# Kernel optimization log

Measured on AMD Instinct MI355X. Metric: run time of the kernel, lower is better.

Reference implementation:

```python
import jax, jax.numpy as jnp
import numpy as np

N_MODULES = 8
AG_HIDDEN = 512
N_HID = 512
OUT_SIZE = 10
BATCH = 8192


def _state_mask(n_modules, n0, n1):
    # torch: eye(M).repeat_interleave(n0, 0).repeat_interleave(n1, 1)
    m = jnp.eye(n_modules, dtype=jnp.float32)
    return jnp.repeat(jnp.repeat(m, n0, axis=0), n1, axis=1)


def setup_inputs() -> dict:
    key = jax.random.key(0)
    ks = jax.random.split(key, 5)
    d_in = N_MODULES * AG_HIDDEN
    d_hid = N_MODULES * N_HID
    d_out = N_MODULES * OUT_SIZE
    s1 = 1.0 / np.sqrt(d_in)
    s2 = 1.0 / np.sqrt(d_hid)
    return {
        "x": jax.random.normal(ks[0], (BATCH, d_in), jnp.float32),
        "W1": jax.random.uniform(ks[1], (d_hid, d_in), jnp.float32, -s1, s1),
        "b1": jax.random.uniform(ks[2], (d_hid,), jnp.float32, -s1, s1),
        "W2": jax.random.uniform(ks[3], (d_out, d_hid), jnp.float32, -s2, s2),
        "b2": jax.random.uniform(ks[4], (d_out,), jnp.float32, -s2, s2),
    }


def reference(x, W1, b1, W2, b2):
    # block-diagonal masks (intra-module connectivity only)
    mask1 = _state_mask(N_MODULES, N_HID, AG_HIDDEN)   # [d_hid, d_in]
    mask2 = _state_mask(N_MODULES, OUT_SIZE, N_HID)    # [d_out, d_hid]
    h = jax.nn.relu(x @ (W1 * mask1).T + b1)           # [B, d_hid]
    y = h @ (W2 * mask2).T + b2                        # [B, d_out]
    # split(OUT_SIZE, -1) then stack on dim 1 == reshape to [B, n_modules, OUT_SIZE]
    return y.reshape(y.shape[0], N_MODULES, OUT_SIZE)
```

## Files before the change

kernel.cpp:

```cpp
#include <hip/hip_runtime.h>


#define NMOD 8
#define DIM 512
#define OSZ 10
#define BATCH 8192
#define D_IN 4096
#define D_OUT 80
#define BM 64
#define BN 256
#define BK 32

typedef __attribute__((ext_vector_type(8))) short short8;
typedef __attribute__((ext_vector_type(4))) float float4v;

__device__ __forceinline__ unsigned short f2bf(float f) {
    unsigned int u = __builtin_bit_cast(unsigned int, f);
    u += 0x7fffu + ((u >> 16) & 1u);
    return (unsigned short)(u >> 16);
}

__device__ __forceinline__ short8 cvt8(float4 a, float4 b) {
    short8 r;
    r[0] = (short)f2bf(a.x); r[1] = (short)f2bf(a.y); r[2] = (short)f2bf(a.z); r[3] = (short)f2bf(a.w);
    r[4] = (short)f2bf(b.x); r[5] = (short)f2bf(b.y); r[6] = (short)f2bf(b.z); r[7] = (short)f2bf(b.w);
    return r;
}

__global__ void init_out_kernel(const float* __restrict__ b2, float* __restrict__ out) {
    int idx = blockIdx.x * 256 + threadIdx.x;
    out[idx] = b2[idx % D_OUT];
}

__global__ void cvt_w_kernel(const float* __restrict__ W1, ushort* __restrict__ w1b) {
    int j = blockIdx.x * 256 + threadIdx.x;
    int mm = j >> 16, rem = j & 65535, r = rem >> 7, c4 = rem & 127;
    float4 v = *(const float4*)(W1 + (size_t)(mm * DIM + r) * D_IN + mm * DIM + c4 * 4);
    *(ushort4*)(w1b + (size_t)mm * DIM * DIM + r * DIM + c4 * 4) =
        make_ushort4(f2bf(v.x), f2bf(v.y), f2bf(v.z), f2bf(v.w));
}

template <bool WPRE>
__global__ __launch_bounds__(256, 3)
void fused_kernel(const float* __restrict__ x, const float* __restrict__ W1,
                  const ushort* __restrict__ w1b, const float* __restrict__ b1,
                  const float* __restrict__ W2, const float* __restrict__ b2,
                  float* __restrict__ out) {
    __shared__ ushort smem[16384];
    ushort* ldsA = smem;
    ushort* ldsB = smem + 2048;
    ushort* ldsH = smem;

    const int tid  = threadIdx.x;
    const int wave = tid >> 6;
    const int lane = tid & 63;
    const int r16  = lane & 15;
    const int kq   = lane >> 4;

    const int bid     = blockIdx.x;
    const int m       = bid & 7;
    const int t2      = bid >> 3;
    const int half    = t2 & 1;
    const int rowBase = (t2 >> 1) * BM;

    const float*  xsrc = x + (size_t)rowBase * D_IN + m * DIM;
    const ushort* w1m  = w1b + (size_t)m * DIM * DIM + (size_t)half * BN * DIM;
    const float*  w1f  = W1 + (size_t)(m * DIM + half * BN) * D_IN + m * DIM;

    float4v acc[4][4];
#pragma unroll
    for (int i = 0; i < 4; i++)
#pragma unroll
        for (int j = 0; j < 4; j++) acc[i][j] = (float4v){0.f, 0.f, 0.f, 0.f};

    const int srow = tid >> 2;
    const int sg   = tid & 3;

    for (int kk = 0; kk < DIM / BK; kk++) {
        const int k0 = kk * BK;
        {
            const int s = (srow >> 1) & 3;
            const float* p = xsrc + (size_t)srow * D_IN + k0 + sg * 8;
            *(short8*)(ldsA + srow * BK + (sg ^ s) * 8) = cvt8(*(const float4*)p, *(const float4*)(p + 4));
        }
        if (WPRE) {
#pragma unroll
            for (int r = 0; r < 4; r++) {
                const int row = r * 64 + srow;
                const int s   = (row >> 1) & 3;
                __builtin_amdgcn_global_load_lds(
                    (const __attribute__((address_space(1))) void*)(w1m + (size_t)row * DIM + k0 + (sg ^ s) * 8),
                    (__attribute__((address_space(3))) void*)(ldsB + row * BK + sg * 8), 16, 0, 0);
            }
        } else {
#pragma unroll
            for (int r = 0; r < 4; r++) {
                const int row = r * 64 + srow;
                const int s   = (row >> 1) & 3;
                const float* p = w1f + (size_t)row * D_IN + k0 + sg * 8;
                *(short8*)(ldsB + row * BK + (sg ^ s) * 8) = cvt8(*(const float4*)p, *(const float4*)(p + 4));
            }
        }
        __syncthreads();

        short8 aF[4], bF[4];
#pragma unroll
        for (int mt = 0; mt < 4; mt++) {
            const int row = mt * 16 + r16;
            aF[mt] = *(const short8*)(ldsA + row * BK + (kq ^ ((row >> 1) & 3)) * 8);
        }
#pragma unroll
        for (int nt = 0; nt < 4; nt++) {
            const int row = wave * 64 + nt * 16 + r16;
            bF[nt] = *(const short8*)(ldsB + row * BK + (kq ^ ((row >> 1) & 3)) * 8);
        }
#pragma unroll
        for (int mt = 0; mt < 4; mt++)
#pragma unroll
            for (int nt = 0; nt < 4; nt++)
                acc[mt][nt] = __builtin_amdgcn_mfma_f32_16x16x32_bf16(aF[mt], bF[nt], acc[mt][nt], 0, 0, 0);
        __syncthreads();
    }

    float b1v[4];
#pragma unroll
    for (int nt = 0; nt < 4; nt++)
        b1v[nt] = b1[m * DIM + half * BN + wave * 64 + nt * 16 + r16];

#pragma unroll
    for (int mt = 0; mt < 4; mt++) {
#pragma unroll
        for (int nt = 0; nt < 4; nt++) {
#pragma unroll
            for (int reg = 0; reg < 4; reg++) {
                float v = acc[mt][nt][reg] + b1v[nt];
                v = v > 0.f ? v : 0.f;
                const int lr  = mt * 16 + kq * 4 + reg;
                const int col = wave * 64 + nt * 16 + r16;
                ldsH[lr * BN + (col ^ ((lr & 7) << 3))] = f2bf(v);
            }
        }
    }
    __syncthreads();

    {
        float4v acc2 = (float4v){0.f, 0.f, 0.f, 0.f};
        const int hrow = wave * 16 + r16;
        const int hsw  = (hrow & 7) << 3;
        const float* w2row = W2 + (size_t)(m * OSZ + r16) * D_IN + m * DIM + half * BN;
#pragma unroll
        for (int kk2 = 0; kk2 < BN / 32; kk2++) {
            const int c = kk2 * 32 + kq * 8;
            short8 ha = *(const short8*)(ldsH + hrow * BN + (c ^ hsw));
            short8 wb = {0, 0, 0, 0, 0, 0, 0, 0};
            if (r16 < OSZ) {
                const float* p = w2row + c;
                wb = cvt8(*(const float4*)p, *(const float4*)(p + 4));
            }
            acc2 = __builtin_amdgcn_mfma_f32_16x16x32_bf16(ha, wb, acc2, 0, 0, 0);
        }
        if (r16 < OSZ) {
#pragma unroll
            for (int reg = 0; reg < 4; reg++) {
                const int grow = rowBase + wave * 16 + kq * 4 + reg;
                atomicAdd(out + (size_t)grow * D_OUT + m * OSZ + r16, acc2[reg]);
            }
        }
    }
}

extern "C" void kernel_launch(void* const* d_in, const int* in_sizes, int n_in,
                              void* d_out, int out_size, void* d_ws, size_t ws_size,
                              hipStream_t stream) {
    const float* x  = (const float*)d_in[0];
    const float* W1 = (const float*)d_in[1];
    const float* b1 = (const float*)d_in[2];
    const float* W2 = (const float*)d_in[3];
    const float* b2 = (const float*)d_in[4];
    float* out = (float*)d_out;

    init_out_kernel<<<dim3(2560), dim3(256), 0, stream>>>(b2, out);

    if (ws_size >= (size_t)NMOD * DIM * DIM * sizeof(ushort)) {
        ushort* w1b = (ushort*)d_ws;
        cvt_w_kernel<<<dim3(2048), dim3(256), 0, stream>>>(W1, w1b);
        fused_kernel<true><<<dim3(2048), dim3(256), 0, stream>>>(x, W1, w1b, b1, W2, b2, out);
    } else {
        fused_kernel<false><<<dim3(2048), dim3(256), 0, stream>>>(x, W1, nullptr, b1, W2, b2, out);
    }
}
```

Before: 269.6 us.

## Keep W1 slice resident in LDS and loop over row tiles per block

Each block now loads a 128x512 slice of its module's W1 block into LDS once, converting it to bf16, and reuses it across four 128-row batch tiles. Only the x tile is streamed, with a register prefetch and a double-buffered LDS stage. This removes the separate W1 conversion pass and the repeated per-block W1 loads, and W2 fragments are held in registers. The cost is about 150KB of LDS per block with 512 threads, which limits occupancy, plus more barriers in the per-tile second-layer epilogue.

```diff
diff --git a/kernel.cpp b/kernel.cpp
--- a/kernel.cpp
+++ b/kernel.cpp
@@ -7,9 +7,16 @@
 #define BATCH 8192
 #define D_IN 4096
 #define D_OUT 80
-#define BM 64
-#define BN 256
+#define QN 128
+#define MT 128
+#define RT 4
 #define BK 32
+
+#define WSTRIDE 520
+#define XSTRIDE 40
+#define HSTRIDE 136
+#define LDSW_SZ 66560
+#define LDSX_SZ 5120
 
 typedef __attribute__((ext_vector_type(8))) short short8;
 typedef __attribute__((ext_vector_type(4))) float float4v;
@@ -32,140 +39,136 @@
     out[idx] = b2[idx % D_OUT];
 }
 
-__global__ void cvt_w_kernel(const float* __restrict__ W1, ushort* __restrict__ w1b) {
-    int j = blockIdx.x * 256 + threadIdx.x;
-    int mm = j >> 16, rem = j & 65535, r = rem >> 7, c4 = rem & 127;
-    float4 v = *(const float4*)(W1 + (size_t)(mm * DIM + r) * D_IN + mm * DIM + c4 * 4);
-    *(ushort4*)(w1b + (size_t)mm * DIM * DIM + r * DIM + c4 * 4) =
-        make_ushort4(f2bf(v.x), f2bf(v.y), f2bf(v.z), f2bf(v.w));
-}
-
-template <bool WPRE>
-__global__ __launch_bounds__(256, 3)
+__global__ __launch_bounds__(512, 2)
 void fused_kernel(const float* __restrict__ x, const float* __restrict__ W1,
-                  const ushort* __restrict__ w1b, const float* __restrict__ b1,
-                  const float* __restrict__ W2, const float* __restrict__ b2,
+                  const float* __restrict__ b1, const float* __restrict__ W2,
                   float* __restrict__ out) {
-    __shared__ ushort smem[16384];
-    ushort* ldsA = smem;
-    ushort* ldsB = smem + 2048;
-    ushort* ldsH = smem;
+    __shared__ ushort smem[76800];
+    ushort* ldsW = smem;
+    ushort* ldsX = smem + LDSW_SZ;
+    ushort* ldsH = smem + LDSW_SZ;
 
     const int tid  = threadIdx.x;
     const int wave = tid >> 6;
     const int lane = tid & 63;
     const int r16  = lane & 15;
     const int kq   = lane >> 4;
+    const int wm   = wave >> 2;
+    const int wn   = wave & 3;
 
-    const int bid     = blockIdx.x;
-    const int m       = bid & 7;
-    const int t2      = bid >> 3;
-    const int half    = t2 & 1;
-    const int rowBase = (t2 >> 1) * BM;
+    const int bid    = blockIdx.x;
+    const int m      = bid & 7;
+    const int q      = (bid >> 3) & 3;
+    const int blkRow = (bid >> 5) * (MT * RT);
 
-    const float*  xsrc = x + (size_t)rowBase * D_IN + m * DIM;
-    const ushort* w1m  = w1b + (size_t)m * DIM * DIM + (size_t)half * BN * DIM;
-    const float*  w1f  = W1 + (size_t)(m * DIM + half * BN) * D_IN + m * DIM;
+    {
+        const int row = tid >> 2, seg = tid & 3;
+        const float* src = W1 + (size_t)(m * DIM + q * QN + row) * D_IN + m * DIM + seg * 128;
+        ushort* dst = ldsW + row * WSTRIDE + seg * 128;
+#pragma unroll 4
+        for (int j = 0; j < 16; j++) {
+            float4 a = *(const float4*)(src + j * 8);
+            float4 b = *(const float4*)(src + j * 8 + 4);
+            *(short8*)(dst + j * 8) = cvt8(a, b);
+        }
+    }
 
-    float4v acc[4][4];
+    short8 w2f[4];
+    {
+        const float* w2base = W2 + (size_t)(m * OSZ + r16) * D_IN + m * DIM + q * QN;
 #pragma unroll
-    for (int i = 0; i < 4; i++)
+        for (int kc = 0; kc < 4; kc++) {
+            if (r16 < OSZ) {
+                const float* p = w2base + (kc * 4 + kq) * 8;
+                w2f[kc] = cvt8(*(const float4*)p, *(const float4*)(p + 4));
+            } else {
+                w2f[kc] = (short8){0, 0, 0, 0, 0, 0, 0, 0};
+            }
+        }
+    }
+
+    float b1v[2];
 #pragma unroll
-        for (int j = 0; j < 4; j++) acc[i][j] = (float4v){0.f, 0.f, 0.f, 0.f};
+    for (int nt = 0; nt < 2; nt++)
+        b1v[nt] = b1[m * DIM + q * QN + wn * 32 + nt * 16 + r16];
 
     const int srow = tid >> 2;
-    const int sg   = tid & 3;
+    const int sc   = tid & 3;
 
-    for (int kk = 0; kk < DIM / BK; kk++) {
-        const int k0 = kk * BK;
+    for (int rt = 0; rt < RT; rt++) {
+        const int rowBase = blkRow + rt * MT;
+        const float* xsrc = x + (size_t)(rowBase + srow) * D_IN + m * DIM + sc * 8;
+
+        float4v acc[4][2];
+#pragma unroll
+        for (int i = 0; i < 4; i++)
+#pragma unroll
+            for (int j = 0; j < 2; j++) acc[i][j] = (float4v){0.f, 0.f, 0.f, 0.f};
+
         {
-            const int s = (srow >> 1) & 3;
-            const float* p = xsrc + (size_t)srow * D_IN + k0 + sg * 8;
-            *(short8*)(ldsA + srow * BK + (sg ^ s) * 8) = cvt8(*(const float4*)p, *(const float4*)(p + 4));
+            float4 a = *(const float4*)(xsrc);
+            float4 b = *(const float4*)(xsrc + 4);
+            *(short8*)(ldsX + srow * XSTRIDE + sc * 8) = cvt8(a, b);
         }
-        if (WPRE) {
+
+        for (int kk = 0; kk < DIM / BK; kk++) {
+            __syncthreads();
+            float4 na, nb;
+            const bool pf = (kk < DIM / BK - 1);
+            if (pf) {
+                const float* p = xsrc + (kk + 1) * BK;
+                na = *(const float4*)p;
+                nb = *(const float4*)(p + 4);
+            }
+            const ushort* xb = ldsX + (kk & 1) * LDSX_SZ;
+            short8 aF[4], bF[2];
 #pragma unroll
-            for (int r = 0; r < 4; r++) {
-                const int row = r * 64 + srow;
-                const int s   = (row >> 1) & 3;
-                __builtin_amdgcn_global_load_lds(
-                    (const __attribute__((address_space(1))) void*)(w1m + (size_t)row * DIM + k0 + (sg ^ s) * 8),
-                    (__attribute__((address_space(3))) void*)(ldsB + row * BK + sg * 8), 16, 0, 0);
+            for (int mt = 0; mt < 4; mt++)
+                aF[mt] = *(const short8*)(xb + (wm * 64 + mt * 16 + r16) * XSTRIDE + kq * 8);
+#pragma unroll
+            for (int nt = 0; nt < 2; nt++)
+                bF[nt] = *(const short8*)(ldsW + (wn * 32 + nt * 16 + r16) * WSTRIDE + (kk * 4 + kq) * 8);
+#pragma unroll
+            for (int mt = 0; mt < 4; mt++)
+#pragma unroll
+                for (int nt = 0; nt < 2; nt++)
+                    acc[mt][nt] = __builtin_amdgcn_mfma_f32_16x16x32_bf16(aF[mt], bF[nt], acc[mt][nt], 0, 0, 0);
+            if (pf)
+                *(short8*)(ldsX + ((kk + 1) & 1) * LDSX_SZ + srow * XSTRIDE + sc * 8) = cvt8(na, nb);
+        }
+
+        for (int hh = 0; hh < 2; hh++) {
+            __syncthreads();
+            if (wm == hh) {
+#pragma unroll
+                for (int mt = 0; mt < 4; mt++)
+#pragma unroll
+                    for (int nt = 0; nt < 2; nt++)
+#pragma unroll
+                        for (int reg = 0; reg < 4; reg++) {
+                            float v = acc[mt][nt][reg] + b1v[nt];
+                            v = v > 0.f ? v : 0.f;
+                            ldsH[(mt * 16 + kq * 4 + reg) * HSTRIDE + wn * 32 + nt * 16 + r16] = f2bf(v);
+                        }
             }
-        } else {
+            __syncthreads();
+            if (wave < 4) {
+                float4v acc2 = (float4v){0.f, 0.f, 0.f, 0.f};
 #pragma unroll
-            for (int r = 0; r < 4; r++) {
-                const int row = r * 64 + srow;
-                const int s   = (row >> 1) & 3;
-                const float* p = w1f + (size_t)row * D_IN + k0 + sg * 8;
-                *(short8*)(ldsB + row * BK + (sg ^ s) * 8) = cvt8(*(const float4*)p, *(const float4*)(p + 4));
+                for (int kc = 0; kc < 4; kc++) {
+                    short8 hA = *(const short8*)(ldsH + (wave * 16 + r16) * HSTRIDE + (kc * 4 + kq) * 8);
+                    acc2 = __builtin_amdgcn_mfma_f32_16x16x32_bf16(hA, w2f[kc], acc2, 0, 0, 0);
+                }
+                if (r16 < OSZ) {
+#pragma unroll
+                    for (int reg = 0; reg < 4; reg++) {
+                        const int grow = rowBase + hh * 64 + wave * 16 + kq * 4 + reg;
+                        atomicAdd(out + (size_t)grow * D_OUT + m * OSZ + r16, acc2[reg]);
+                    }
+                }
             }
         }
         __syncthreads();
-
-        short8 aF[4], bF[4];
-#pragma unroll
-        for (int mt = 0; mt < 4; mt++) {
-            const int row = mt * 16 + r16;
-            aF[mt] = *(const short8*)(ldsA + row * BK + (kq ^ ((row >> 1) & 3)) * 8);
-        }
-#pragma unroll
-        for (int nt = 0; nt < 4; nt++) {
-            const int row = wave * 64 + nt * 16 + r16;
-            bF[nt] = *(const short8*)(ldsB + row * BK + (kq ^ ((row >> 1) & 3)) * 8);
-        }
-#pragma unroll
-        for (int mt = 0; mt < 4; mt++)
-#pragma unroll
-            for (int nt = 0; nt < 4; nt++)
-                acc[mt][nt] = __builtin_amdgcn_mfma_f32_16x16x32_bf16(aF[mt], bF[nt], acc[mt][nt], 0, 0, 0);
-        __syncthreads();
-    }
-
-    float b1v[4];
-#pragma unroll
-    for (int nt = 0; nt < 4; nt++)
-        b1v[nt] = b1[m * DIM + half * BN + wave * 64 + nt * 16 + r16];
-
-#pragma unroll
-    for (int mt = 0; mt < 4; mt++) {
-#pragma unroll
-        for (int nt = 0; nt < 4; nt++) {
-#pragma unroll
-            for (int reg = 0; reg < 4; reg++) {
-                float v = acc[mt][nt][reg] + b1v[nt];
-                v = v > 0.f ? v : 0.f;
-                const int lr  = mt * 16 + kq * 4 + reg;
-                const int col = wave * 64 + nt * 16 + r16;
-                ldsH[lr * BN + (col ^ ((lr & 7) << 3))] = f2bf(v);
-            }
-        }
-    }
-    __syncthreads();
-
-    {
-        float4v acc2 = (float4v){0.f, 0.f, 0.f, 0.f};
-        const int hrow = wave * 16 + r16;
-        const int hsw  = (hrow & 7) << 3;
-        const float* w2row = W2 + (size_t)(m * OSZ + r16) * D_IN + m * DIM + half * BN;
-#pragma unroll
-        for (int kk2 = 0; kk2 < BN / 32; kk2++) {
-            const int c = kk2 * 32 + kq * 8;
-            short8 ha = *(const short8*)(ldsH + hrow * BN + (c ^ hsw));
-            short8 wb = {0, 0, 0, 0, 0, 0, 0, 0};
-            if (r16 < OSZ) {
-                const float* p = w2row + c;
-                wb = cvt8(*(const float4*)p, *(const float4*)(p + 4));
-            }
-            acc2 = __builtin_amdgcn_mfma_f32_16x16x32_bf16(ha, wb, acc2, 0, 0, 0);
-        }
-        if (r16 < OSZ) {
-#pragma unroll
-            for (int reg = 0; reg < 4; reg++) {
-                const int grow = rowBase + wave * 16 + kq * 4 + reg;
-                atomicAdd(out + (size_t)grow * D_OUT + m * OSZ + r16, acc2[reg]);
-            }
-        }
     }
 }
 
@@ -180,12 +183,5 @@
     float* out = (float*)d_out;
 
     init_out_kernel<<<dim3(2560), dim3(256), 0, stream>>>(b2, out);
-
-    if (ws_size >= (size_t)NMOD * DIM * DIM * sizeof(ushort)) {
-        ushort* w1b = (ushort*)d_ws;
-        cvt_w_kernel<<<dim3(2048), dim3(256), 0, stream>>>(W1, w1b);
-        fused_kernel<true><<<dim3(2048), dim3(256), 0, stream>>>(x, W1, w1b, b1, W2, b2, out);
-    } else {
-        fused_kernel<false><<<dim3(2048), dim3(256), 0, stream>>>(x, W1, nullptr, b1, W2, b2, out);
-    }
+    fused_kernel<<<dim3(512), dim3(512), 0, stream>>>(x, W1, b1, W2, out);
 }
```

New measurement: 327.2 us. 1.21x slower.

## Double-buffer LDS tiles and double the row tile to 128

Applied to the files above, without the earlier changes.

Doubles the batch rows per block from 64 to 128, which halves the grid and doubles the reuse of each W1 tile. It also double-buffers the A and B tiles in LDS, so the next k-step's loads are issued while the current MFMAs run, with one barrier per iteration. The A tile and the hidden buffer switch from XOR swizzling to padded strides. The cost is higher register pressure (acc[8][4]), occupancy lowered to 2 blocks, and more LDS per block.

```diff
diff --git a/kernel.cpp b/kernel.cpp
--- a/kernel.cpp
+++ b/kernel.cpp
@@ -7,9 +7,14 @@
 #define BATCH 8192
 #define D_IN 4096
 #define D_OUT 80
-#define BM 64
+#define BM 128
 #define BN 256
 #define BK 32
+
+#define ASTRIDE 40
+#define HSTRIDE 264
+#define LDSA_SZ 5120
+#define LDSB_SZ 8192
 
 typedef __attribute__((ext_vector_type(8))) short short8;
 typedef __attribute__((ext_vector_type(4))) float float4v;
@@ -41,15 +46,17 @@
 }
 
 template <bool WPRE>
-__global__ __launch_bounds__(256, 3)
+__global__ __launch_bounds__(256, 2)
 void fused_kernel(const float* __restrict__ x, const float* __restrict__ W1,
                   const ushort* __restrict__ w1b, const float* __restrict__ b1,
                   const float* __restrict__ W2, const float* __restrict__ b2,
                   float* __restrict__ out) {
-    __shared__ ushort smem[16384];
-    ushort* ldsA = smem;
-    ushort* ldsB = smem + 2048;
-    ushort* ldsH = smem;
+    __shared__ __attribute__((aligned(16))) ushort smem[26624];
+    ushort* ldsA0 = smem;
+    ushort* ldsA1 = smem + LDSA_SZ;
+    ushort* ldsB0 = smem + 2 * LDSA_SZ;
+    ushort* ldsB1 = smem + 2 * LDSA_SZ + LDSB_SZ;
+    ushort* ldsH  = smem;
 
     const int tid  = threadIdx.x;
     const int wave = tid >> 6;
@@ -59,67 +66,104 @@
 
     const int bid     = blockIdx.x;
     const int m       = bid & 7;
-    const int t2      = bid >> 3;
-    const int half    = t2 & 1;
-    const int rowBase = (t2 >> 1) * BM;
+    const int half    = (bid >> 3) & 1;
+    const int rowBase = (bid >> 4) * BM;
 
     const float*  xsrc = x + (size_t)rowBase * D_IN + m * DIM;
-    const ushort* w1m  = w1b + (size_t)m * DIM * DIM + (size_t)half * BN * DIM;
+    const ushort* w1h  = w1b + (size_t)m * DIM * DIM + (size_t)half * BN * DIM;
     const float*  w1f  = W1 + (size_t)(m * DIM + half * BN) * D_IN + m * DIM;
 
-    float4v acc[4][4];
-#pragma unroll
-    for (int i = 0; i < 4; i++)
+    const int arow = tid >> 1;
+    const int ah   = tid & 1;
+    const int brow = tid >> 2;
+    const int bc   = tid & 3;
+
+    float4v acc[8][4];
+#pragma unroll
+    for (int i = 0; i < 8; i++)
 #pragma unroll
         for (int j = 0; j < 4; j++) acc[i][j] = (float4v){0.f, 0.f, 0.f, 0.f};
 
-    const int srow = tid >> 2;
-    const int sg   = tid & 3;
+    if (WPRE) {
+#pragma unroll
+        for (int r = 0; r < 4; r++) {
+            const int row = r * 64 + brow;
+            const int f   = (row >> 1) & 3;
+            __builtin_amdgcn_global_load_lds(
+                (const __attribute__((address_space(1))) void*)(w1h + (size_t)row * DIM + (bc ^ f) * 8),
+                (__attribute__((address_space(3))) void*)(ldsB0 + row * BK + bc * 8), 16, 0, 0);
+        }
+    } else {
+#pragma unroll
+        for (int r = 0; r < 4; r++) {
+            const int row = r * 64 + brow;
+            const int f   = (row >> 1) & 3;
+            const float* p = w1f + (size_t)row * D_IN + bc * 8;
+            *(short8*)(ldsB0 + row * BK + (bc ^ f) * 8) = cvt8(*(const float4*)p, *(const float4*)(p + 4));
+        }
+    }
+    {
+        const float* p = xsrc + (size_t)arow * D_IN + ah * 16;
+        float4 a0 = *(const float4*)p, a1 = *(const float4*)(p + 4);
+        float4 a2 = *(const float4*)(p + 8), a3 = *(const float4*)(p + 12);
+        *(short8*)(ldsA0 + arow * ASTRIDE + ah * 16)     = cvt8(a0, a1);
+        *(short8*)(ldsA0 + arow * ASTRIDE + ah * 16 + 8) = cvt8(a2, a3);
+    }
 
     for (int kk = 0; kk < DIM / BK; kk++) {
-        const int k0 = kk * BK;
-        {
-            const int s = (srow >> 1) & 3;
-            const float* p = xsrc + (size_t)srow * D_IN + k0 + sg * 8;
-            *(short8*)(ldsA + srow * BK + (sg ^ s) * 8) = cvt8(*(const float4*)p, *(const float4*)(p + 4));
-        }
-        if (WPRE) {
-#pragma unroll
-            for (int r = 0; r < 4; r++) {
-                const int row = r * 64 + srow;
-                const int s   = (row >> 1) & 3;
-                __builtin_amdgcn_global_load_lds(
-                    (const __attribute__((address_space(1))) void*)(w1m + (size_t)row * DIM + k0 + (sg ^ s) * 8),
-                    (__attribute__((address_space(3))) void*)(ldsB + row * BK + sg * 8), 16, 0, 0);
-            }
-        } else {
-#pragma unroll
-            for (int r = 0; r < 4; r++) {
-                const int row = r * 64 + srow;
-                const int s   = (row >> 1) & 3;
-                const float* p = w1f + (size_t)row * D_IN + k0 + sg * 8;
-                *(short8*)(ldsB + row * BK + (sg ^ s) * 8) = cvt8(*(const float4*)p, *(const float4*)(p + 4));
-            }
-        }
         __syncthreads();
-
-        short8 aF[4], bF[4];
-#pragma unroll
-        for (int mt = 0; mt < 4; mt++) {
-            const int row = mt * 16 + r16;
-            aF[mt] = *(const short8*)(ldsA + row * BK + (kq ^ ((row >> 1) & 3)) * 8);
-        }
+        ushort* Ac = (kk & 1) ? ldsA1 : ldsA0;
+        ushort* Bc = (kk & 1) ? ldsB1 : ldsB0;
+        ushort* An = (kk & 1) ? ldsA0 : ldsA1;
+        ushort* Bn = (kk & 1) ? ldsB0 : ldsB1;
+
+        float4 xr0, xr1, xr2, xr3;
+        const bool pf = (kk < DIM / BK - 1);
+        if (pf) {
+            const int k0n = (kk + 1) * BK;
+            if (WPRE) {
+#pragma unroll
+                for (int r = 0; r < 4; r++) {
+                    const int row = r * 64 + brow;
+                    const int f   = (row >> 1) & 3;
+                    __builtin_amdgcn_global_load_lds(
+                        (const __attribute__((address_space(1))) void*)(w1h + (size_t)row * DIM + k0n + (bc ^ f) * 8),
+                        (__attribute__((address_space(3))) void*)(Bn + row * BK + bc * 8), 16, 0, 0);
+                }
+            }
+            const float* p = xsrc + (size_t)arow * D_IN + kk * BK + BK + ah * 16;
+            xr0 = *(const float4*)p;     xr1 = *(const float4*)(p + 4);
+            xr2 = *(const float4*)(p + 8); xr3 = *(const float4*)(p + 12);
+        }
+
+        short8 aF[8], bF[4];
+#pragma unroll
+        for (int mt = 0; mt < 8; mt++)
+            aF[mt] = *(const short8*)(Ac + (mt * 16 + r16) * ASTRIDE + kq * 8);
 #pragma unroll
         for (int nt = 0; nt < 4; nt++) {
             const int row = wave * 64 + nt * 16 + r16;
-            bF[nt] = *(const short8*)(ldsB + row * BK + (kq ^ ((row >> 1) & 3)) * 8);
-        }
-#pragma unroll
-        for (int mt = 0; mt < 4; mt++)
+            bF[nt] = *(const short8*)(Bc + row * BK + (kq ^ ((row >> 1) & 3)) * 8);
+        }
+#pragma unroll
+        for (int mt = 0; mt < 8; mt++)
 #pragma unroll
             for (int nt = 0; nt < 4; nt++)
                 acc[mt][nt] = __builtin_amdgcn_mfma_f32_16x16x32_bf16(aF[mt], bF[nt], acc[mt][nt], 0, 0, 0);
-        __syncthreads();
+
+        if (pf) {
+            *(short8*)(An + arow * ASTRIDE + ah * 16)     = cvt8(xr0, xr1);
+            *(short8*)(An + arow * ASTRIDE + ah * 16 + 8) = cvt8(xr2, xr3);
+            if (!WPRE) {
+#pragma unroll
+                for (int r = 0; r < 4; r++) {
+                    const int row = r * 64 + brow;
+                    const int f   = (row >> 1) & 3;
+                    const float* p = w1f + (size_t)row * D_IN + kk * BK + BK + bc * 8;
+                    *(short8*)(Bn + row * BK + (bc ^ f) * 8) = cvt8(*(const float4*)p, *(const float4*)(p + 4));
+                }
+            }
+        }
     }
 
     float b1v[4];
@@ -127,43 +171,46 @@
     for (int nt = 0; nt < 4; nt++)
         b1v[nt] = b1[m * DIM + half * BN + wave * 64 + nt * 16 + r16];
 
-#pragma unroll
-    for (int mt = 0; mt < 4; mt++) {
-#pragma unroll
-        for (int nt = 0; nt < 4; nt++) {
-#pragma unroll
-            for (int reg = 0; reg < 4; reg++) {
-                float v = acc[mt][nt][reg] + b1v[nt];
-                v = v > 0.f ? v : 0.f;
-                const int lr  = mt * 16 + kq * 4 + reg;
-                const int col = wave * 64 + nt * 16 + r16;
-                ldsH[lr * BN + (col ^ ((lr & 7) << 3))] = f2bf(v);
-            }
-        }
-    }
-    __syncthreads();
-
-    {
-        float4v acc2 = (float4v){0.f, 0.f, 0.f, 0.f};
-        const int hrow = wave * 16 + r16;
-        const int hsw  = (hrow & 7) << 3;
-        const float* w2row = W2 + (size_t)(m * OSZ + r16) * D_IN + m * DIM + half * BN;
-#pragma unroll
-        for (int kk2 = 0; kk2 < BN / 32; kk2++) {
-            const int c = kk2 * 32 + kq * 8;
-            short8 ha = *(const short8*)(ldsH + hrow * BN + (c ^ hsw));
-            short8 wb = {0, 0, 0, 0, 0, 0, 0, 0};
+    for (int hh = 0; hh < 2; hh++) {
+        __syncthreads();
+#pragma unroll
+        for (int mt2 = 0; mt2 < 4; mt2++) {
+            const int mt = hh * 4 + mt2;
+#pragma unroll
+            for (int nt = 0; nt < 4; nt++) {
+#pragma unroll
+                for (int reg = 0; reg < 4; reg++) {
+                    float v = acc[mt][nt][reg] + b1v[nt];
+                    v = v > 0.f ? v : 0.f;
+                    const int lr  = mt2 * 16 + kq * 4 + reg;
+                    const int col = wave * 64 + nt * 16 + r16;
+                    ldsH[lr * HSTRIDE + col] = f2bf(v);
+                }
+            }
+        }
+        __syncthreads();
+
+        {
+            float4v acc2 = (float4v){0.f, 0.f, 0.f, 0.f};
+            const int hrow = wave * 16 + r16;
+            const float* w2row = W2 + (size_t)(m * OSZ + r16) * D_IN + m * DIM + half * BN;
+#pragma unroll
+            for (int kc = 0; kc < BN / 32; kc++) {
+                const int c = kc * 32 + kq * 8;
+                short8 hA = *(const short8*)(ldsH + hrow * HSTRIDE + c);
+                short8 wb = {0, 0, 0, 0, 0, 0, 0, 0};
+                if (r16 < OSZ) {
+                    const float* p = w2row + c;
+                    wb = cvt8(*(const float4*)p, *(const float4*)(p + 4));
+                }
+                acc2 = __builtin_amdgcn_mfma_f32_16x16x32_bf16(hA, wb, acc2, 0, 0, 0);
+            }
             if (r16 < OSZ) {
-                const float* p = w2row + c;
-                wb = cvt8(*(const float4*)p, *(const float4*)(p + 4));
-            }
-            acc2 = __builtin_amdgcn_mfma_f32_16x16x32_bf16(ha, wb, acc2, 0, 0, 0);
-        }
-        if (r16 < OSZ) {
-#pragma unroll
-            for (int reg = 0; reg < 4; reg++) {
-                const int grow = rowBase + wave * 16 + kq * 4 + reg;
-                atomicAdd(out + (size_t)grow * D_OUT + m * OSZ + r16, acc2[reg]);
+#pragma unroll
+                for (int reg = 0; reg < 4; reg++) {
+                    const int grow = rowBase + hh * 64 + wave * 16 + kq * 4 + reg;
+                    atomicAdd(out + (size_t)grow * D_OUT + m * OSZ + r16, acc2[reg]);
+                }
             }
         }
     }
@@ -184,8 +231,8 @@
     if (ws_size >= (size_t)NMOD * DIM * DIM * sizeof(ushort)) {
         ushort* w1b = (ushort*)d_ws;
         cvt_w_kernel<<<dim3(2048), dim3(256), 0, stream>>>(W1, w1b);
-        fused_kernel<true><<<dim3(2048), dim3(256), 0, stream>>>(x, W1, w1b, b1, W2, b2, out);
+        fused_kernel<true><<<dim3(1024), dim3(256), 0, stream>>>(x, W1, w1b, b1, W2, b2, out);
     } else {
-        fused_kernel<false><<<dim3(2048), dim3(256), 0, stream>>>(x, W1, nullptr, b1, W2, b2, out);
-    }
-}
+        fused_kernel<false><<<dim3(1024), dim3(256), 0, stream>>>(x, W1, nullptr, b1, W2, b2, out);
+    }
+}
```

New measurement: 259.0 us. -3.9%, faster.
